# Performance work log

Measured on AMD Instinct MI355X. Metric: run time of the kernel, lower is better.

The kernel has to match this reference:

```python
import jax, jax.numpy as jnp
import numpy as np

B, L, E = 16, 192, 128
T = 25  # hardcoded self.season_len in the original module


def setup_inputs() -> dict:
    key = jax.random.key(0)
    kx, kw, kb = jax.random.split(key, 3)
    x = jax.random.normal(kx, (B, L, E), dtype=jnp.float32)
    # nn.Linear(1, 2): weight [2,1], bias [2]
    W = jax.random.normal(kw, (2, 1), dtype=jnp.float32)
    b = jax.random.normal(kb, (2,), dtype=jnp.float32)
    return {"x": x, "W": W, "b": b}


def reference(x, W, b):
    # x: [B, L, E]. Faithful to the torch forward:
    #   for i <= T: append x[:, i:i+1, :]                 -> [B,1,E]
    #   for i >  T: append sum(stack(x_i, x_{i-T}) * softmax(Linear(x[...,None])), -1)
    #               which broadcasts to a full [B,L,E] block (softmax over the
    #               2-way Linear output is identical for every i, so compute once).
    Bb, Ll, Ee = x.shape
    logits = x[..., None] * W[:, 0] + b                # [B,L,E,2]
    s = jax.nn.softmax(logits, axis=-1)                # [B,L,E,2]
    idx = jnp.arange(T + 1, Ll)                        # i = 26 .. L-1  (M = L-26)
    xi = x[:, idx, :]                                  # [B,M,E]  x[:, i, :]
    xp = x[:, idx - T, :]                              # [B,M,E]  x[:, i-T, :]
    # blocks[b,i,l,e] = xi[b,i,e]*s[b,l,e,0] + xp[b,i,e]*s[b,l,e,1]
    blocks = (xi[:, :, None, :] * s[:, None, :, :, 0]
              + xp[:, :, None, :] * s[:, None, :, :, 1])  # [B,M,L,E]
    blocks = blocks.reshape(Bb, -1, Ee)                # [B, M*L, E]
    # loop order: i=0..T first (identity rows), then the big blocks in order
    return jnp.concatenate([x[:, :T + 1, :], blocks], axis=1)  # [B, T+1 + M*L, E]
```

## Files before the change

### kernel.cpp

```cpp
#include <hip/hip_runtime.h>

constexpr int Bn = 16;
constexpr int L  = 192;
constexpr int E  = 128;
constexpr int T  = 25;
constexpr int NI = L - T - 1;
constexpr int ROWS_OUT = (T + 1) + NI * L;
constexpr int E4 = E / 4;
constexpr int S_ELEMS = Bn * L * E;
constexpr int PLANE_F4 = L * E4;

typedef float f4 __attribute__((ext_vector_type(4)));

__global__ __launch_bounds__(256) void sigmoid_kernel(
    const float* __restrict__ x,
    const float* __restrict__ W,
    const float* __restrict__ bv,
    float* __restrict__ s)
{
    const int g = blockIdx.x * 256 + threadIdx.x;
    if (g >= S_ELEMS / 4) return;
    const float dw = W[1] - W[0];
    const float db = bv[1] - bv[0];
    const f4 xv = ((const f4*)x)[g];
    f4 o;
    o.x = __builtin_amdgcn_rcpf(1.0f + __expf(fmaf(xv.x, dw, db)));
    o.y = __builtin_amdgcn_rcpf(1.0f + __expf(fmaf(xv.y, dw, db)));
    o.z = __builtin_amdgcn_rcpf(1.0f + __expf(fmaf(xv.z, dw, db)));
    o.w = __builtin_amdgcn_rcpf(1.0f + __expf(fmaf(xv.w, dw, db)));
    ((f4*)s)[g] = o;
}

__global__ __launch_bounds__(256) void blocks_kernel(
    const float* __restrict__ x,
    const float* __restrict__ s,
    float* __restrict__ out)
{
    const int blk = blockIdx.x;
    const int t = threadIdx.x;

    if (blk < Bn * NI) {
        const int b = blk / NI;
        const int i = blk % NI;
        const int e4 = t & (E4 - 1);

        const f4* __restrict__ xrow_i = (const f4*)(x + ((size_t)(b * L + T + 1 + i)) * E);
        const f4* __restrict__ xrow_p = (const f4*)(x + ((size_t)(b * L + 1 + i)) * E);
        const f4 xp4 = xrow_p[e4];
        const f4 xi4 = xrow_i[e4];
        const f4 d4 = xi4 - xp4;

        const f4* __restrict__ sp = (const f4*)(s) + (size_t)b * PLANE_F4;
        f4* __restrict__ ob = (f4*)(out) + ((size_t)b * ROWS_OUT + (T + 1) + (size_t)i * L) * E4;

        #pragma unroll 4
        for (int k = 0; k < PLANE_F4 / 256; ++k) {
            const int j = k * 256 + t;
            const f4 s4 = sp[j];
            f4 o;
            o.x = fmaf(d4.x, s4.x, xp4.x);
            o.y = fmaf(d4.y, s4.y, xp4.y);
            o.z = fmaf(d4.z, s4.z, xp4.z);
            o.w = fmaf(d4.w, s4.w, xp4.w);
            __builtin_nontemporal_store(o, &ob[j]);
        }
    } else {
        const int gid = (blk - Bn * NI) * 256 + t;
        constexpr int per_b = (T + 1) * E4;
        constexpr int total = Bn * per_b;
        if (gid < total) {
            const int b = gid / per_b;
            const int r = gid % per_b;
            const f4* __restrict__ xb = (const f4*)(x + (size_t)b * L * E);
            f4* __restrict__ ob = (f4*)(out + (size_t)b * ROWS_OUT * E);
            __builtin_nontemporal_store(xb[r], &ob[r]);
        }
    }
}

__global__ __launch_bounds__(256) void blocks_kernel_inline(
    const float* __restrict__ x,
    const float* __restrict__ W,
    const float* __restrict__ bv,
    float* __restrict__ out)
{
    const int blk = blockIdx.x;
    const int t = threadIdx.x;
    const float dw = W[1] - W[0];
    const float db = bv[1] - bv[0];

    if (blk < Bn * NI) {
        const int b = blk / NI;
        const int i = blk % NI;
        const int e4 = t & (E4 - 1);

        const f4* __restrict__ xrow_i = (const f4*)(x + ((size_t)(b * L + T + 1 + i)) * E);
        const f4* __restrict__ xrow_p = (const f4*)(x + ((size_t)(b * L + 1 + i)) * E);
        const f4 xp4 = xrow_p[e4];
        const f4 xi4 = xrow_i[e4];
        const f4 d4 = xi4 - xp4;

        const f4* __restrict__ xp_plane = (const f4*)(x) + (size_t)b * PLANE_F4;
        f4* __restrict__ ob = (f4*)(out) + ((size_t)b * ROWS_OUT + (T + 1) + (size_t)i * L) * E4;

        for (int k = 0; k < PLANE_F4 / 256; ++k) {
            const int j = k * 256 + t;
            const f4 xv = xp_plane[j];
            f4 o;
            o.x = fmaf(d4.x, __builtin_amdgcn_rcpf(1.0f + __expf(fmaf(xv.x, dw, db))), xp4.x);
            o.y = fmaf(d4.y, __builtin_amdgcn_rcpf(1.0f + __expf(fmaf(xv.y, dw, db))), xp4.y);
            o.z = fmaf(d4.z, __builtin_amdgcn_rcpf(1.0f + __expf(fmaf(xv.z, dw, db))), xp4.z);
            o.w = fmaf(d4.w, __builtin_amdgcn_rcpf(1.0f + __expf(fmaf(xv.w, dw, db))), xp4.w);
            __builtin_nontemporal_store(o, &ob[j]);
        }
    } else {
        const int gid = (blk - Bn * NI) * 256 + t;
        constexpr int per_b = (T + 1) * E4;
        constexpr int total = Bn * per_b;
        if (gid < total) {
            const int b = gid / per_b;
            const int r = gid % per_b;
            const f4* __restrict__ xb = (const f4*)(x + (size_t)b * L * E);
            f4* __restrict__ ob = (f4*)(out + (size_t)b * ROWS_OUT * E);
            __builtin_nontemporal_store(xb[r], &ob[r]);
        }
    }
}

extern "C" void kernel_launch(void* const* d_in, const int* in_sizes, int n_in,
                              void* d_out, int out_size, void* d_ws, size_t ws_size,
                              hipStream_t stream) {
    const float* x  = (const float*)d_in[0];
    const float* W  = (const float*)d_in[1];
    const float* bv = (const float*)d_in[2];
    float* out = (float*)d_out;

    constexpr int prefix_f4 = Bn * (T + 1) * E4;
    constexpr int prefix_blocks = (prefix_f4 + 255) / 256;
    const int grid2 = Bn * NI + prefix_blocks;

    if (ws_size >= (size_t)S_ELEMS * sizeof(float)) {
        float* s = (float*)d_ws;
        sigmoid_kernel<<<(S_ELEMS / 4 + 255) / 256, 256, 0, stream>>>(x, W, bv, s);
        blocks_kernel<<<grid2, 256, 0, stream>>>(x, s, out);
    } else {
        blocks_kernel_inline<<<grid2, 256, 0, stream>>>(x, W, bv, out);
    }
}
```

Measured before the change: 266.1 us.

## Fuse sigmoid and block expansion into one grid-stride flat-index kernel

Result: no change. 270.0 us (+1.5%).

```diff
diff --git a/kernel.cpp b/kernel.cpp
--- a/kernel.cpp
+++ b/kernel.cpp
@@ -7,122 +7,52 @@
 constexpr int NI = L - T - 1;
 constexpr int ROWS_OUT = (T + 1) + NI * L;
 constexpr int E4 = E / 4;
-constexpr int S_ELEMS = Bn * L * E;
-constexpr int PLANE_F4 = L * E4;
+constexpr int PREF_PER_B = (T + 1) * E4;
+
+constexpr unsigned BODY_F4  = (unsigned)Bn * NI * L * E4;
+constexpr unsigned PREF_F4  = (unsigned)Bn * PREF_PER_B;
+constexpr unsigned TOTAL_F4 = BODY_F4 + PREF_F4;
 
 typedef float f4 __attribute__((ext_vector_type(4)));
 
-__global__ __launch_bounds__(256) void sigmoid_kernel(
-    const float* __restrict__ x,
-    const float* __restrict__ W,
-    const float* __restrict__ bv,
-    float* __restrict__ s)
-{
-    const int g = blockIdx.x * 256 + threadIdx.x;
-    if (g >= S_ELEMS / 4) return;
-    const float dw = W[1] - W[0];
-    const float db = bv[1] - bv[0];
-    const f4 xv = ((const f4*)x)[g];
-    f4 o;
-    o.x = __builtin_amdgcn_rcpf(1.0f + __expf(fmaf(xv.x, dw, db)));
-    o.y = __builtin_amdgcn_rcpf(1.0f + __expf(fmaf(xv.y, dw, db)));
-    o.z = __builtin_amdgcn_rcpf(1.0f + __expf(fmaf(xv.z, dw, db)));
-    o.w = __builtin_amdgcn_rcpf(1.0f + __expf(fmaf(xv.w, dw, db)));
-    ((f4*)s)[g] = o;
-}
-
-__global__ __launch_bounds__(256) void blocks_kernel(
-    const float* __restrict__ x,
-    const float* __restrict__ s,
-    float* __restrict__ out)
-{
-    const int blk = blockIdx.x;
-    const int t = threadIdx.x;
-
-    if (blk < Bn * NI) {
-        const int b = blk / NI;
-        const int i = blk % NI;
-        const int e4 = t & (E4 - 1);
-
-        const f4* __restrict__ xrow_i = (const f4*)(x + ((size_t)(b * L + T + 1 + i)) * E);
-        const f4* __restrict__ xrow_p = (const f4*)(x + ((size_t)(b * L + 1 + i)) * E);
-        const f4 xp4 = xrow_p[e4];
-        const f4 xi4 = xrow_i[e4];
-        const f4 d4 = xi4 - xp4;
-
-        const f4* __restrict__ sp = (const f4*)(s) + (size_t)b * PLANE_F4;
-        f4* __restrict__ ob = (f4*)(out) + ((size_t)b * ROWS_OUT + (T + 1) + (size_t)i * L) * E4;
-
-        #pragma unroll 4
-        for (int k = 0; k < PLANE_F4 / 256; ++k) {
-            const int j = k * 256 + t;
-            const f4 s4 = sp[j];
-            f4 o;
-            o.x = fmaf(d4.x, s4.x, xp4.x);
-            o.y = fmaf(d4.y, s4.y, xp4.y);
-            o.z = fmaf(d4.z, s4.z, xp4.z);
-            o.w = fmaf(d4.w, s4.w, xp4.w);
-            __builtin_nontemporal_store(o, &ob[j]);
-        }
-    } else {
-        const int gid = (blk - Bn * NI) * 256 + t;
-        constexpr int per_b = (T + 1) * E4;
-        constexpr int total = Bn * per_b;
-        if (gid < total) {
-            const int b = gid / per_b;
-            const int r = gid % per_b;
-            const f4* __restrict__ xb = (const f4*)(x + (size_t)b * L * E);
-            f4* __restrict__ ob = (f4*)(out + (size_t)b * ROWS_OUT * E);
-            __builtin_nontemporal_store(xb[r], &ob[r]);
-        }
-    }
-}
-
-__global__ __launch_bounds__(256) void blocks_kernel_inline(
+__global__ __launch_bounds__(256, 6) void fused_kernel(
     const float* __restrict__ x,
     const float* __restrict__ W,
     const float* __restrict__ bv,
     float* __restrict__ out)
 {
-    const int blk = blockIdx.x;
-    const int t = threadIdx.x;
     const float dw = W[1] - W[0];
     const float db = bv[1] - bv[0];
+    const f4* __restrict__ xv4 = (const f4*)x;
+    f4* __restrict__ ov4 = (f4*)out;
 
-    if (blk < Bn * NI) {
-        const int b = blk / NI;
-        const int i = blk % NI;
-        const int e4 = t & (E4 - 1);
+    const unsigned stride = gridDim.x * 256u;
+    for (unsigned g = blockIdx.x * 256u + threadIdx.x; g < TOTAL_F4; g += stride) {
+        if (g < BODY_F4) {
+            const unsigned e4   = g & (E4 - 1);
+            const unsigned rest = g >> 5;
+            const unsigned l    = rest % L;
+            const unsigned bi   = rest / L;
+            const unsigned i    = bi % NI;
+            const unsigned b    = bi / NI;
 
-        const f4* __restrict__ xrow_i = (const f4*)(x + ((size_t)(b * L + T + 1 + i)) * E);
-        const f4* __restrict__ xrow_p = (const f4*)(x + ((size_t)(b * L + 1 + i)) * E);
-        const f4 xp4 = xrow_p[e4];
-        const f4 xi4 = xrow_i[e4];
-        const f4 d4 = xi4 - xp4;
+            const f4 xv = xv4[(b * L + l) * E4 + e4];
+            const f4 xp = xv4[(b * L + 1 + i) * E4 + e4];
+            const f4 xi = xv4[(b * L + T + 1 + i) * E4 + e4];
 
-        const f4* __restrict__ xp_plane = (const f4*)(x) + (size_t)b * PLANE_F4;
-        f4* __restrict__ ob = (f4*)(out) + ((size_t)b * ROWS_OUT + (T + 1) + (size_t)i * L) * E4;
+            f4 o;
+            o.x = fmaf(xi.x - xp.x, __builtin_amdgcn_rcpf(1.0f + __expf(fmaf(xv.x, dw, db))), xp.x);
+            o.y = fmaf(xi.y - xp.y, __builtin_amdgcn_rcpf(1.0f + __expf(fmaf(xv.y, dw, db))), xp.y);
+            o.z = fmaf(xi.z - xp.z, __builtin_amdgcn_rcpf(1.0f + __expf(fmaf(xv.z, dw, db))), xp.z);
+            o.w = fmaf(xi.w - xp.w, __builtin_amdgcn_rcpf(1.0f + __expf(fmaf(xv.w, dw, db))), xp.w);
 
-        for (int k = 0; k < PLANE_F4 / 256; ++k) {
-            const int j = k * 256 + t;
-            const f4 xv = xp_plane[j];
-            f4 o;
-            o.x = fmaf(d4.x, __builtin_amdgcn_rcpf(1.0f + __expf(fmaf(xv.x, dw, db))), xp4.x);
-            o.y = fmaf(d4.y, __builtin_amdgcn_rcpf(1.0f + __expf(fmaf(xv.y, dw, db))), xp4.y);
-            o.z = fmaf(d4.z, __builtin_amdgcn_rcpf(1.0f + __expf(fmaf(xv.z, dw, db))), xp4.z);
-            o.w = fmaf(d4.w, __builtin_amdgcn_rcpf(1.0f + __expf(fmaf(xv.w, dw, db))), xp4.w);
-            __builtin_nontemporal_store(o, &ob[j]);
-        }
-    } else {
-        const int gid = (blk - Bn * NI) * 256 + t;
-        constexpr int per_b = (T + 1) * E4;
-        constexpr int total = Bn * per_b;
-        if (gid < total) {
-            const int b = gid / per_b;
-            const int r = gid % per_b;
-            const f4* __restrict__ xb = (const f4*)(x + (size_t)b * L * E);
-            f4* __restrict__ ob = (f4*)(out + (size_t)b * ROWS_OUT * E);
-            __builtin_nontemporal_store(xb[r], &ob[r]);
+            __builtin_nontemporal_store(o, &ov4[g + (b + 1u) * PREF_PER_B]);
+        } else {
+            const unsigned p = g - BODY_F4;
+            const unsigned b = p / PREF_PER_B;
+            const unsigned r = p % PREF_PER_B;
+            const f4 v = xv4[b * (L * E4) + r];
+            __builtin_nontemporal_store(v, &ov4[(size_t)b * (ROWS_OUT * E4) + r]);
         }
     }
 }
@@ -135,15 +65,6 @@
     const float* bv = (const float*)d_in[2];
     float* out = (float*)d_out;
 
-    constexpr int prefix_f4 = Bn * (T + 1) * E4;
-    constexpr int prefix_blocks = (prefix_f4 + 255) / 256;
-    const int grid2 = Bn * NI + prefix_blocks;
-
-    if (ws_size >= (size_t)S_ELEMS * sizeof(float)) {
-        float* s = (float*)d_ws;
-        sigmoid_kernel<<<(S_ELEMS / 4 + 255) / 256, 256, 0, stream>>>(x, W, bv, s);
-        blocks_kernel<<<grid2, 256, 0, stream>>>(x, s, out);
-    } else {
-        blocks_kernel_inline<<<grid2, 256, 0, stream>>>(x, W, bv, out);
-    }
+    const int grid = 2048;
+    fused_kernel<<<grid, 256, 0, stream>>>(x, W, bv, out);
 }
```
